# Kernel tuning notes

Hardware: AMD Instinct MI355X
Metric: run time of the kernel (lower is better)

The kernel has to match this reference:

```python
import jax, jax.numpy as jnp
import numpy as np

B, L, D, H = 2, 2048, 1024, 16
DH = D // H  # per-head dim = 64


def setup_inputs() -> dict:
    key = jax.random.key(0)
    ks = jax.random.split(key, 7)
    s = 1.0 / np.sqrt(D)
    x = jax.random.normal(ks[0], (B, L, D), dtype=jnp.float32)
    Wq = jax.random.normal(ks[1], (D, D), dtype=jnp.float32) * s
    bq = jax.random.normal(ks[2], (D,), dtype=jnp.float32) * s
    Wk = jax.random.normal(ks[3], (D, D), dtype=jnp.float32) * s
    bk = jax.random.normal(ks[4], (D,), dtype=jnp.float32) * s
    Wv = jax.random.normal(ks[5], (D, D), dtype=jnp.float32) * s
    bv = jax.random.normal(ks[6], (D,), dtype=jnp.float32) * s
    # strict upper-triangular causal mask; mask==1 means position is masked (-inf)
    atten_mask = jnp.triu(jnp.ones((L, L), dtype=jnp.int32), k=1)
    return {"x": x, "atten_mask": atten_mask, "Wq": Wq, "bq": bq,
            "Wk": Wk, "bk": bk, "Wv": Wv, "bv": bv}


def reference(x, atten_mask, Wq, bq, Wk, bk, Wv, bv):
    # nn.Linear: y = x @ W^T + b
    q = x @ Wq.T + bq  # [B,L,D]
    k = x @ Wk.T + bk
    v = x @ Wv.T + bv
    # contiguous split into heads == reshape to [B,L,H,DH]
    q = q.reshape(B, L, H, DH)
    k = k.reshape(B, L, H, DH)
    v = v.reshape(B, L, H, DH)
    scale = jnp.sqrt(jnp.float32(DH))
    scores = jnp.einsum('blhd,bmhd->bhlm', q, k) / scale  # [B,H,L,L]
    # torch.where(mask == 1, -inf, scores)
    scores = jnp.where(atten_mask[None, None] == 1, -jnp.inf, scores)
    attn = jax.nn.softmax(scores, axis=-1)
    out = jnp.einsum('bhlm,bmhd->blhd', attn, v)  # [B,L,H,DH]
    return out.reshape(B, L, D)  # concat heads along channel dim
```

## Files before the change

kernel.cpp:

```cpp
#include <hip/hip_runtime.h>
#include <hip/hip_bf16.h>

#define BDIM 2
#define LSEQ 2048
#define DMODEL 1024
#define NH 16
#define DHEAD 64
#define CTS 136

typedef __bf16 bf16_t;
typedef __attribute__((ext_vector_type(8))) __bf16 bf16x8;
typedef __attribute__((ext_vector_type(4))) __bf16 bf16x4;
typedef __attribute__((ext_vector_type(2))) __bf16 bf16x2;
typedef __attribute__((ext_vector_type(4))) float f32x4;
typedef __attribute__((ext_vector_type(4))) int i32x4;

static __device__ __forceinline__ f32x4 mfma16(bf16x8 a, bf16x8 b, f32x4 c) {
    return __builtin_amdgcn_mfma_f32_16x16x32_bf16(a, b, c, 0, 0, 0);
}

static __device__ __forceinline__ void load_lds16(const bf16_t* g, void* l) {
    __builtin_amdgcn_global_load_lds(
        (const __attribute__((address_space(1))) void*)g,
        (__attribute__((address_space(3))) void*)l, 16, 0, 0);
}

__global__ void convert_all(
    const float* __restrict__ x,
    const float* __restrict__ Wq, const float* __restrict__ Wk, const float* __restrict__ Wv,
    const float* __restrict__ bq, const float* __restrict__ bk, const float* __restrict__ bv,
    bf16_t* __restrict__ cx,
    bf16_t* __restrict__ cWq, bf16_t* __restrict__ cWk, bf16_t* __restrict__ cWv,
    bf16_t* __restrict__ cbq, bf16_t* __restrict__ cbk, bf16_t* __restrict__ cbv,
    float SQ)
{
    const int blk = blockIdx.x;
    const float* src; bf16_t* dst; int base, cnt; float sc = 1.0f;
    if (blk < 1024)      { src = x;  dst = cx;  base = blk * 1024;          cnt = 1024; }
    else if (blk < 1280) { src = Wq; dst = cWq; base = (blk - 1024) * 1024; cnt = 1024; sc = SQ; }
    else if (blk < 1536) { src = Wk; dst = cWk; base = (blk - 1280) * 1024; cnt = 1024; }
    else if (blk < 1792) { src = Wv; dst = cWv; base = (blk - 1536) * 1024; cnt = 1024; }
    else if (blk == 1792){ src = bq; dst = cbq; base = 0; cnt = 256; sc = SQ; }
    else if (blk == 1793){ src = bk; dst = cbk; base = 0; cnt = 256; }
    else                 { src = bv; dst = cbv; base = 0; cnt = 256; }

    for (int i = base + threadIdx.x; i < base + cnt; i += 256) {
        f32x4 v = *(const f32x4*)(src + 4 * (size_t)i);
        bf16x4 o;
        o[0] = (bf16_t)(v[0] * sc); o[1] = (bf16_t)(v[1] * sc);
        o[2] = (bf16_t)(v[2] * sc); o[3] = (bf16_t)(v[3] * sc);
        *(bf16x4*)(dst + 4 * (size_t)i) = o;
    }
}

__global__ __launch_bounds__(256) void qkv_gemm(
    const bf16_t* __restrict__ x,
    const bf16_t* __restrict__ W0, const bf16_t* __restrict__ W1, const bf16_t* __restrict__ W2,
    const bf16_t* __restrict__ b0, const bf16_t* __restrict__ b1, const bf16_t* __restrict__ b2,
    bf16_t* __restrict__ yq, bf16_t* __restrict__ yk, bf16_t* __restrict__ yvT)
{
    __shared__ alignas(16) char smem[128 * CTS * 2];
    bf16_t* At = (bf16_t*)smem;
    bf16_t* Bt = At + 128 * 64;
    bf16_t* Ct = (bf16_t*)smem;

    const int tid  = threadIdx.x;
    const int lane = tid & 63;
    const int w    = tid >> 6;
    const int quad = lane >> 4;
    const int n16  = lane & 15;
    const int lane3 = lane >> 3;
    const int lane7 = lane & 7;
    const int swz8  = (lane7 ^ lane3) * 8;

    const int m0 = blockIdx.y * 128;
    const int n0 = blockIdx.x * 128;
    const int z  = blockIdx.z;

    const bf16_t* W    = (z == 0) ? W0 : ((z == 1) ? W1 : W2);
    const bf16_t* bias = (z == 0) ? b0 : ((z == 1) ? b1 : b2);

    const int wm = (w >> 1) * 64;
    const int wn = (w & 1) * 64;

    f32x4 acc[4][4] = {};

    const bf16_t* gx = x + (size_t)(m0 + 32 * w + lane3) * DMODEL + swz8;
    const bf16_t* gw = W + (size_t)(n0 + 32 * w + lane3) * DMODEL + swz8;
    char* lA = (char*)At + w * 4096;
    char* lB = (char*)Bt + w * 4096;

    const int swz = n16 & 7;

    for (int k0 = 0; k0 < DMODEL; k0 += 64) {
        #pragma unroll
        for (int ii = 0; ii < 4; ++ii) {
            load_lds16(gx + (size_t)(8 * ii) * DMODEL + k0, lA + ii * 1024);
            load_lds16(gw + (size_t)(8 * ii) * DMODEL + k0, lB + ii * 1024);
        }
        __syncthreads();

        #pragma unroll
        for (int kk = 0; kk < 2; ++kk) {
            bf16x8 af[4], bfv[4];
            #pragma unroll
            for (int mt = 0; mt < 4; ++mt) {
                const bf16_t* ar = At + (wm + mt * 16 + n16) * 64;
                af[mt] = *(const bf16x8*)(ar + (((quad + 4 * kk)) ^ swz) * 8);
            }
            #pragma unroll
            for (int nt = 0; nt < 4; ++nt) {
                const bf16_t* br = Bt + (wn + nt * 16 + n16) * 64;
                bfv[nt] = *(const bf16x8*)(br + (((quad + 4 * kk)) ^ swz) * 8);
            }
            #pragma unroll
            for (int mt = 0; mt < 4; ++mt)
                #pragma unroll
                for (int nt = 0; nt < 4; ++nt)
                    acc[mt][nt] = mfma16(af[mt], bfv[nt], acc[mt][nt]);
        }
        __syncthreads();
    }

    if (z < 2) {
        bf16_t* y = (z == 0) ? yq : yk;
        #pragma unroll
        for (int nt = 0; nt < 4; ++nt) {
            int jc = wn + nt * 16 + n16;
            float bv = (float)bias[n0 + jc];
            #pragma unroll
            for (int mt = 0; mt < 4; ++mt) {
                int rr = wm + mt * 16 + quad * 4;
                #pragma unroll
                for (int r = 0; r < 4; ++r)
                    Ct[(rr + r) * CTS + jc] = (bf16_t)(acc[mt][nt][r] + bv);
            }
        }
        __syncthreads();
        const int l    = tid >> 1;
        const int half = tid & 1;
        const int hh   = (n0 >> 6) + half;
        const int i    = m0 + l;
        const int bb   = i >> 11, ll = i & 2047;
        bf16_t* dst = &y[(((size_t)bb * NH + hh) * LSEQ + ll) * DHEAD];
        const bf16_t* srcr = &Ct[l * CTS + half * 64];
        #pragma unroll
        for (int c = 0; c < 8; ++c)
            *(bf16x8*)(dst + c * 8) = *(const bf16x8*)(srcr + c * 8);
    } else {
        #pragma unroll
        for (int nt = 0; nt < 4; ++nt) {
            int j = n0 + wn + nt * 16 + n16;
            float bv = (float)bias[j];
            #pragma unroll
            for (int mt = 0; mt < 4; ++mt) {
                int i0 = m0 + wm + mt * 16 + quad * 4;
                int bb = i0 >> 11, l = i0 & 2047;
                bf16x4 pk;
                #pragma unroll
                for (int r = 0; r < 4; ++r) pk[r] = (bf16_t)(acc[mt][nt][r] + bv);
                *(bf16x4*)(&yvT[((size_t)bb * DMODEL + j) * LSEQ + l]) = pk;
            }
        }
    }
}

__global__ __launch_bounds__(256) void attn_fused(
    const bf16_t* __restrict__ qp,
    const bf16_t* __restrict__ kp,
    const bf16_t* __restrict__ vtp,
    float* __restrict__ out,
    float* __restrict__ Opart,
    float* __restrict__ ml)
{
    __shared__ alignas(16) bf16_t Ks[2][64 * 64];
    __shared__ alignas(16) bf16_t Vs[2][64 * 64];

    const int tid  = threadIdx.x;
    const int lane = tid & 63;
    const int w    = tid >> 6;
    const int quad = lane >> 4;
    const int n16  = lane & 15;
    const int lane3 = lane >> 3;
    const int lane7 = lane & 7;
    const int swz8  = (lane7 ^ lane3) * 8;
    const int swz   = n16 & 7;

    const int bh  = blockIdx.x;
    const int yy  = blockIdx.y;
    const int p   = yy & 15;
    const bool isA = (yy < 16);
    const int b = bh >> 4, h = bh & 15;
    const int row = w * 16 + n16;
    const size_t hb = (size_t)bh * (LSEQ * DHEAD);

    float m_, l_;
    f32x4 oacc[4];

    auto process = [&](int qt, int t0, int ntiles, bool maskLast) {
        const int iq = qt * 64 + row;
        const bf16_t* qq = qp + hb + (size_t)iq * DHEAD;
        const bf16x8 qb0 = *(const bf16x8*)(qq + quad * 8);
        const bf16x8 qb1 = *(const bf16x8*)(qq + 32 + quad * 8);

        const bf16_t* gk = kp  + hb + (size_t)(t0 * 64 + 16 * w + lane3) * DHEAD + swz8;
        const bf16_t* gv = vtp + hb + (size_t)(16 * w + lane3) * LSEQ + t0 * 64 + swz8;

        int buf = 0;
        {
            char* lk = (char*)&Ks[0][0] + w * 2048;
            char* lv = (char*)&Vs[0][0] + w * 2048;
            load_lds16(gk,              lk);
            load_lds16(gk + 8 * DHEAD,  lk + 1024);
            load_lds16(gv,              lv);
            load_lds16(gv + 8 * LSEQ,   lv + 1024);
            gk += 64 * DHEAD; gv += 64;
        }
        __syncthreads();

        for (int it = 0; it < ntiles; ++it) {
            if (it + 1 < ntiles) {
                char* lk = (char*)&Ks[buf ^ 1][0] + w * 2048;
                char* lv = (char*)&Vs[buf ^ 1][0] + w * 2048;
                load_lds16(gk,              lk);
                load_lds16(gk + 8 * DHEAD,  lk + 1024);
                load_lds16(gv,              lv);
                load_lds16(gv + 8 * LSEQ,   lv + 1024);
                gk += 64 * DHEAD; gv += 64;
            }

            const bf16_t* kb = &Ks[buf][0];
            f32x4 s[4];
            #pragma unroll
            for (int t = 0; t < 4; ++t) {
                const bf16_t* krow = kb + (t * 16 + n16) * 64;
                bf16x8 k0v = *(const bf16x8*)(krow + ((quad    ) ^ swz) * 8);
                bf16x8 k1v = *(const bf16x8*)(krow + ((quad + 4) ^ swz) * 8);
                f32x4 z = {0.f, 0.f, 0.f, 0.f};
                z = mfma16(k0v, qb0, z);
                z = mfma16(k1v, qb1, z);
                s[t] = z;
            }

            if (maskLast && it == ntiles - 1) {
                const int k0 = (t0 + it) * 64;
                #pragma unroll
                for (int t = 0; t < 4; ++t)
                    #pragma unroll
                    for (int r = 0; r < 4; ++r)
                        if (k0 + t * 16 + quad * 4 + r > iq) s[t][r] = -1e30f;
            }

            float mx = -1e30f;
            #pragma unroll
            for (int t = 0; t < 4; ++t)
                mx = fmaxf(mx, fmaxf(fmaxf(s[t][0], s[t][1]), fmaxf(s[t][2], s[t][3])));
            mx = fmaxf(mx, __shfl_xor(mx, 16, 64));
            mx = fmaxf(mx, __shfl_xor(mx, 32, 64));
            const float mnew  = fmaxf(m_, mx);
            const float alpha = __builtin_amdgcn_exp2f(m_ - mnew);
            m_ = mnew;

            float rs = 0.f;
            int pr[4][2];
            #pragma unroll
            for (int t = 0; t < 4; ++t) {
                float p0 = __builtin_amdgcn_exp2f(s[t][0] - mnew);
                float p1 = __builtin_amdgcn_exp2f(s[t][1] - mnew);
                float p2 = __builtin_amdgcn_exp2f(s[t][2] - mnew);
                float p3 = __builtin_amdgcn_exp2f(s[t][3] - mnew);
                rs += (p0 + p1) + (p2 + p3);
                bf16x2 a; a[0] = (bf16_t)p0; a[1] = (bf16_t)p1;
                bf16x2 c; c[0] = (bf16_t)p2; c[1] = (bf16_t)p3;
                pr[t][0] = __builtin_bit_cast(int, a);
                pr[t][1] = __builtin_bit_cast(int, c);
            }
            rs += __shfl_xor(rs, 16, 64);
            rs += __shfl_xor(rs, 32, 64);
            l_ = l_ * alpha + rs;
            #pragma unroll
            for (int t = 0; t < 4; ++t) {
                oacc[t][0] *= alpha; oacc[t][1] *= alpha;
                oacc[t][2] *= alpha; oacc[t][3] *= alpha;
            }

            const bf16_t* vbs = &Vs[buf][0];
            #pragma unroll
            for (int c = 0; c < 2; ++c) {
                int frag[4];
                #pragma unroll
                for (int pi = 0; pi < 4; ++pi) {
                    int srcl = ((((quad & 1) * 2) + (pi >> 1)) * 16 + n16) * 4;
                    int vA = __builtin_amdgcn_ds_bpermute(srcl, pr[2 * c][pi & 1]);
                    int vB = __builtin_amdgcn_ds_bpermute(srcl, pr[2 * c + 1][pi & 1]);
                    frag[pi] = (quad < 2) ? vA : vB;
                }
                i32x4 fv = {frag[0], frag[1], frag[2], frag[3]};
                bf16x8 pb = __builtin_bit_cast(bf16x8, fv);

                #pragma unroll
                for (int t = 0; t < 4; ++t) {
                    const bf16_t* vrow = vbs + (t * 16 + n16) * 64;
                    bf16x8 va = *(const bf16x8*)(vrow + ((quad + 4 * c) ^ swz) * 8);
                    oacc[t] = mfma16(va, pb, oacc[t]);
                }
            }

            __syncthreads();
            buf ^= 1;
        }
    };

    if (isA) {
        m_ = -1e30f; l_ = 0.f;
        #pragma unroll
        for (int t = 0; t < 4; ++t) { f32x4 zz = {0.f,0.f,0.f,0.f}; oacc[t] = zz; }
        process(p, 0, p + 1, true);
        {
            const float inv = 1.0f / l_;
            const int iq = p * 64 + row;
            float* orow = out + ((size_t)b * LSEQ + iq) * DMODEL + h * DHEAD;
            #pragma unroll
            for (int t = 0; t < 4; ++t) {
                f32x4 o;
                o[0] = oacc[t][0] * inv; o[1] = oacc[t][1] * inv;
                o[2] = oacc[t][2] * inv; o[3] = oacc[t][3] * inv;
                *(f32x4*)(orow + t * 16 + quad * 4) = o;
            }
        }
        m_ = -1e30f; l_ = 0.f;
        #pragma unroll
        for (int t = 0; t < 4; ++t) { f32x4 zz = {0.f,0.f,0.f,0.f}; oacc[t] = zz; }
        process(31 - p, 0, 16 - p, false);
        {
            const int pidx = (bh * 16 + (15 - p)) * 2 + 0;
            float* Ob = Opart + (size_t)pidx * 4096 + row * 64;
            #pragma unroll
            for (int t = 0; t < 4; ++t)
                *(f32x4*)(Ob + t * 16 + quad * 4) = oacc[t];
            if (quad == 0) {
                ml[(size_t)pidx * 128 + row * 2]     = m_;
                ml[(size_t)pidx * 128 + row * 2 + 1] = l_;
            }
        }
    } else {
        m_ = -1e30f; l_ = 0.f;
        #pragma unroll
        for (int t = 0; t < 4; ++t) { f32x4 zz = {0.f,0.f,0.f,0.f}; oacc[t] = zz; }
        process(31 - p, 16 - p, 16, true);
        {
            const int pidx = (bh * 16 + (15 - p)) * 2 + 1;
            float* Ob = Opart + (size_t)pidx * 4096 + row * 64;
            #pragma unroll
            for (int t = 0; t < 4; ++t)
                *(f32x4*)(Ob + t * 16 + quad * 4) = oacc[t];
            if (quad == 0) {
                ml[(size_t)pidx * 128 + row * 2]     = m_;
                ml[(size_t)pidx * 128 + row * 2 + 1] = l_;
            }
        }
    }
}

__global__ __launch_bounds__(256) void attn_combine(
    const float* __restrict__ Opart, const float* __restrict__ ml,
    float* __restrict__ out)
{
    const int bh  = blockIdx.x;
    const int q16 = blockIdx.y;
    const int t   = threadIdx.x;
    const int row = t >> 2;
    const int dh0 = (t & 3) * 16;
    const int p0  = (bh * 16 + q16) * 2;
    const int b = bh >> 4, h = bh & 15;

    float m0 = ml[(size_t)p0 * 128 + row * 2];
    float l0 = ml[(size_t)p0 * 128 + row * 2 + 1];
    float m1 = ml[(size_t)(p0 + 1) * 128 + row * 2];
    float l1 = ml[(size_t)(p0 + 1) * 128 + row * 2 + 1];
    float m  = fmaxf(m0, m1);
    float a0 = __builtin_amdgcn_exp2f(m0 - m);
    float a1 = __builtin_amdgcn_exp2f(m1 - m);
    float inv = 1.0f / (a0 * l0 + a1 * l1);
    a0 *= inv; a1 *= inv;

    const float* P0 = Opart + (size_t)p0 * 4096 + row * 64 + dh0;
    const float* P1 = P0 + 4096;
    float* orow = out + ((size_t)b * LSEQ + ((16 + q16) * 64 + row)) * DMODEL
                + h * DHEAD + dh0;
    #pragma unroll
    for (int c = 0; c < 4; ++c) {
        f32x4 o0 = *(const f32x4*)(P0 + 4 * c);
        f32x4 o1 = *(const f32x4*)(P1 + 4 * c);
        f32x4 o;
        o[0] = a0 * o0[0] + a1 * o1[0];
        o[1] = a0 * o0[1] + a1 * o1[1];
        o[2] = a0 * o0[2] + a1 * o1[2];
        o[3] = a0 * o0[3] + a1 * o1[3];
        *(f32x4*)(orow + 4 * c) = o;
    }
}

extern "C" void kernel_launch(void* const* d_in, const int* in_sizes, int n_in,
                              void* d_out, int out_size, void* d_ws, size_t ws_size,
                              hipStream_t stream)
{
    const float* x  = (const float*)d_in[0];
    const float* Wq = (const float*)d_in[2];
    const float* bq = (const float*)d_in[3];
    const float* Wk = (const float*)d_in[4];
    const float* bk = (const float*)d_in[5];
    const float* Wv = (const float*)d_in[6];
    const float* bv = (const float*)d_in[7];
    float* out = (float*)d_out;

    char* ws = (char*)d_ws;
    bf16_t* q   = (bf16_t*)(ws);
    bf16_t* k   = (bf16_t*)(ws + 8u  * 1024 * 1024);
    bf16_t* vT  = (bf16_t*)(ws + 16u * 1024 * 1024);
    bf16_t* cx  = (bf16_t*)(ws + 24u * 1024 * 1024);
    bf16_t* cWq = (bf16_t*)(ws + 32u * 1024 * 1024);
    bf16_t* cWk = (bf16_t*)(ws + 34u * 1024 * 1024);
    bf16_t* cWv = (bf16_t*)(ws + 36u * 1024 * 1024);
    bf16_t* cbq = (bf16_t*)(ws + 38u * 1024 * 1024);
    bf16_t* cbk = (bf16_t*)(ws + 38u * 1024 * 1024 + 4096);
    bf16_t* cbv = (bf16_t*)(ws + 38u * 1024 * 1024 + 8192);
    float*  mlp = (float*) (ws + 39u * 1024 * 1024);
    float*  Op  = (float*) (ws + 40u * 1024 * 1024);

    const float SQ = 0.125f * 1.44269504088896f;

    convert_all<<<1795, 256, 0, stream>>>(x, Wq, Wk, Wv, bq, bk, bv,
                                          cx, cWq, cWk, cWv, cbq, cbk, cbv, SQ);

    dim3 g1(DMODEL / 128, (BDIM * LSEQ) / 128, 3);
    qkv_gemm<<<g1, 256, 0, stream>>>(cx, cWq, cWk, cWv, cbq, cbk, cbv, q, k, vT);

    dim3 g2(BDIM * NH, 32, 1);
    attn_fused<<<g2, 256, 0, stream>>>(q, k, vT, out, Op, mlp);

    dim3 g3(BDIM * NH, 16, 1);
    attn_combine<<<g3, 256, 0, stream>>>(Op, mlp, out);
}
```

Measured before the change: 193.2 us.

## Enlarge attention query tile to 128 rows so each K/V tile serves two groups

Each wave now handles two 16-row query groups, which doubles the query tile per block from 64 to 128 rows. Every K/V tile loaded into LDS, and every K/V fragment read from it, is reused for twice as many MFMAs, cutting K/V traffic per unit of work. The causal split and the combine kernel are reworked for 128-row tiles, and masking now covers the last two KV tiles. The trade-off is half as many blocks (512 instead of 1024) and higher register pressure from doubled accumulators, which may lower occupancy and load balance on a 256-CU part.

```diff
diff --git a/kernel.cpp b/kernel.cpp
--- a/kernel.cpp
+++ b/kernel.cpp
@@ -188,20 +188,24 @@
 
     const int bh  = blockIdx.x;
     const int yy  = blockIdx.y;
-    const int p   = yy & 15;
-    const bool isA = (yy < 16);
+    const int p   = yy & 7;
+    const bool isA = (yy < 8);
     const int b = bh >> 4, h = bh & 15;
-    const int row = w * 16 + n16;
     const size_t hb = (size_t)bh * (LSEQ * DHEAD);
 
-    float m_, l_;
-    f32x4 oacc[4];
-
-    auto process = [&](int qt, int t0, int ntiles, bool maskLast) {
-        const int iq = qt * 64 + row;
-        const bf16_t* qq = qp + hb + (size_t)iq * DHEAD;
-        const bf16x8 qb0 = *(const bf16x8*)(qq + quad * 8);
-        const bf16x8 qb1 = *(const bf16x8*)(qq + 32 + quad * 8);
+    float m_[2], l_[2];
+    f32x4 oacc[2][4];
+
+    auto process = [&](int qt, int t0, int ntiles, bool maskTail) {
+        int iqg[2];
+        bf16x8 qb[2][2];
+        #pragma unroll
+        for (int g = 0; g < 2; ++g) {
+            iqg[g] = qt * 128 + 32 * w + 16 * g + n16;
+            const bf16_t* qq = qp + hb + (size_t)iqg[g] * DHEAD;
+            qb[g][0] = *(const bf16x8*)(qq + quad * 8);
+            qb[g][1] = *(const bf16x8*)(qq + 32 + quad * 8);
+        }
 
         const bf16_t* gk = kp  + hb + (size_t)(t0 * 64 + 16 * w + lane3) * DHEAD + swz8;
         const bf16_t* gv = vtp + hb + (size_t)(16 * w + lane3) * LSEQ + t0 * 64 + swz8;
@@ -210,10 +214,10 @@
         {
             char* lk = (char*)&Ks[0][0] + w * 2048;
             char* lv = (char*)&Vs[0][0] + w * 2048;
-            load_lds16(gk,              lk);
-            load_lds16(gk + 8 * DHEAD,  lk + 1024);
-            load_lds16(gv,              lv);
-            load_lds16(gv + 8 * LSEQ,   lv + 1024);
+            load_lds16(gk,             lk);
+            load_lds16(gk + 8 * DHEAD, lk + 1024);
+            load_lds16(gv,             lv);
+            load_lds16(gv + 8 * LSEQ,  lv + 1024);
             gk += 64 * DHEAD; gv += 64;
         }
         __syncthreads();
@@ -222,87 +226,101 @@
             if (it + 1 < ntiles) {
                 char* lk = (char*)&Ks[buf ^ 1][0] + w * 2048;
                 char* lv = (char*)&Vs[buf ^ 1][0] + w * 2048;
-                load_lds16(gk,              lk);
-                load_lds16(gk + 8 * DHEAD,  lk + 1024);
-                load_lds16(gv,              lv);
-                load_lds16(gv + 8 * LSEQ,   lv + 1024);
+                load_lds16(gk,             lk);
+                load_lds16(gk + 8 * DHEAD, lk + 1024);
+                load_lds16(gv,             lv);
+                load_lds16(gv + 8 * LSEQ,  lv + 1024);
                 gk += 64 * DHEAD; gv += 64;
             }
 
             const bf16_t* kb = &Ks[buf][0];
-            f32x4 s[4];
+            f32x4 s[2][4];
             #pragma unroll
             for (int t = 0; t < 4; ++t) {
                 const bf16_t* krow = kb + (t * 16 + n16) * 64;
                 bf16x8 k0v = *(const bf16x8*)(krow + ((quad    ) ^ swz) * 8);
                 bf16x8 k1v = *(const bf16x8*)(krow + ((quad + 4) ^ swz) * 8);
-                f32x4 z = {0.f, 0.f, 0.f, 0.f};
-                z = mfma16(k0v, qb0, z);
-                z = mfma16(k1v, qb1, z);
-                s[t] = z;
-            }
-
-            if (maskLast && it == ntiles - 1) {
+                #pragma unroll
+                for (int g = 0; g < 2; ++g) {
+                    f32x4 z = {0.f, 0.f, 0.f, 0.f};
+                    z = mfma16(k0v, qb[g][0], z);
+                    z = mfma16(k1v, qb[g][1], z);
+                    s[g][t] = z;
+                }
+            }
+
+            if (maskTail && it >= ntiles - 2) {
                 const int k0 = (t0 + it) * 64;
                 #pragma unroll
+                for (int g = 0; g < 2; ++g)
+                    #pragma unroll
+                    for (int t = 0; t < 4; ++t)
+                        #pragma unroll
+                        for (int r = 0; r < 4; ++r)
+                            if (k0 + t * 16 + quad * 4 + r > iqg[g]) s[g][t][r] = -1e30f;
+            }
+
+            bf16x8 pb[2][2];
+            #pragma unroll
+            for (int g = 0; g < 2; ++g) {
+                float mx = -1e30f;
+                #pragma unroll
                 for (int t = 0; t < 4; ++t)
+                    mx = fmaxf(mx, fmaxf(fmaxf(s[g][t][0], s[g][t][1]),
+                                         fmaxf(s[g][t][2], s[g][t][3])));
+                mx = fmaxf(mx, __shfl_xor(mx, 16, 64));
+                mx = fmaxf(mx, __shfl_xor(mx, 32, 64));
+                const float mnew  = fmaxf(m_[g], mx);
+                const float alpha = __builtin_amdgcn_exp2f(m_[g] - mnew);
+                m_[g] = mnew;
+
+                float rs = 0.f;
+                int pr[4][2];
+                #pragma unroll
+                for (int t = 0; t < 4; ++t) {
+                    float p0 = __builtin_amdgcn_exp2f(s[g][t][0] - mnew);
+                    float p1 = __builtin_amdgcn_exp2f(s[g][t][1] - mnew);
+                    float p2 = __builtin_amdgcn_exp2f(s[g][t][2] - mnew);
+                    float p3 = __builtin_amdgcn_exp2f(s[g][t][3] - mnew);
+                    rs += (p0 + p1) + (p2 + p3);
+                    bf16x2 a; a[0] = (bf16_t)p0; a[1] = (bf16_t)p1;
+                    bf16x2 c; c[0] = (bf16_t)p2; c[1] = (bf16_t)p3;
+                    pr[t][0] = __builtin_bit_cast(int, a);
+                    pr[t][1] = __builtin_bit_cast(int, c);
+                }
+                rs += __shfl_xor(rs, 16, 64);
+                rs += __shfl_xor(rs, 32, 64);
+                l_[g] = l_[g] * alpha + rs;
+                #pragma unroll
+                for (int t = 0; t < 4; ++t) {
+                    oacc[g][t][0] *= alpha; oacc[g][t][1] *= alpha;
+                    oacc[g][t][2] *= alpha; oacc[g][t][3] *= alpha;
+                }
+
+                #pragma unroll
+                for (int c = 0; c < 2; ++c) {
+                    int frag[4];
                     #pragma unroll
-                    for (int r = 0; r < 4; ++r)
-                        if (k0 + t * 16 + quad * 4 + r > iq) s[t][r] = -1e30f;
-            }
-
-            float mx = -1e30f;
-            #pragma unroll
-            for (int t = 0; t < 4; ++t)
-                mx = fmaxf(mx, fmaxf(fmaxf(s[t][0], s[t][1]), fmaxf(s[t][2], s[t][3])));
-            mx = fmaxf(mx, __shfl_xor(mx, 16, 64));
-            mx = fmaxf(mx, __shfl_xor(mx, 32, 64));
-            const float mnew  = fmaxf(m_, mx);
-            const float alpha = __builtin_amdgcn_exp2f(m_ - mnew);
-            m_ = mnew;
-
-            float rs = 0.f;
-            int pr[4][2];
-            #pragma unroll
-            for (int t = 0; t < 4; ++t) {
-                float p0 = __builtin_amdgcn_exp2f(s[t][0] - mnew);
-                float p1 = __builtin_amdgcn_exp2f(s[t][1] - mnew);
-                float p2 = __builtin_amdgcn_exp2f(s[t][2] - mnew);
-                float p3 = __builtin_amdgcn_exp2f(s[t][3] - mnew);
-                rs += (p0 + p1) + (p2 + p3);
-                bf16x2 a; a[0] = (bf16_t)p0; a[1] = (bf16_t)p1;
-                bf16x2 c; c[0] = (bf16_t)p2; c[1] = (bf16_t)p3;
-                pr[t][0] = __builtin_bit_cast(int, a);
-                pr[t][1] = __builtin_bit_cast(int, c);
-            }
-            rs += __shfl_xor(rs, 16, 64);
-            rs += __shfl_xor(rs, 32, 64);
-            l_ = l_ * alpha + rs;
-            #pragma unroll
-            for (int t = 0; t < 4; ++t) {
-                oacc[t][0] *= alpha; oacc[t][1] *= alpha;
-                oacc[t][2] *= alpha; oacc[t][3] *= alpha;
+                    for (int pi = 0; pi < 4; ++pi) {
+                        int srcl = ((((quad & 1) * 2) + (pi >> 1)) * 16 + n16) * 4;
+                        int vA = __builtin_amdgcn_ds_bpermute(srcl, pr[2 * c][pi & 1]);
+                        int vB = __builtin_amdgcn_ds_bpermute(srcl, pr[2 * c + 1][pi & 1]);
+                        frag[pi] = (quad < 2) ? vA : vB;
+                    }
+                    i32x4 fv = {frag[0], frag[1], frag[2], frag[3]};
+                    pb[g][c] = __builtin_bit_cast(bf16x8, fv);
+                }
             }
 
             const bf16_t* vbs = &Vs[buf][0];
             #pragma unroll
             for (int c = 0; c < 2; ++c) {
-                int frag[4];
-                #pragma unroll
-                for (int pi = 0; pi < 4; ++pi) {
-                    int srcl = ((((quad & 1) * 2) + (pi >> 1)) * 16 + n16) * 4;
-                    int vA = __builtin_amdgcn_ds_bpermute(srcl, pr[2 * c][pi & 1]);
-                    int vB = __builtin_amdgcn_ds_bpermute(srcl, pr[2 * c + 1][pi & 1]);
-                    frag[pi] = (quad < 2) ? vA : vB;
-                }
-                i32x4 fv = {frag[0], frag[1], frag[2], frag[3]};
-                bf16x8 pb = __builtin_bit_cast(bf16x8, fv);
-
                 #pragma unroll
                 for (int t = 0; t < 4; ++t) {
                     const bf16_t* vrow = vbs + (t * 16 + n16) * 64;
                     bf16x8 va = *(const bf16x8*)(vrow + ((quad + 4 * c) ^ swz) * 8);
-                    oacc[t] = mfma16(va, pb, oacc[t]);
+                    oacc[0][t] = mfma16(va, pb[0][c], oacc[0][t]);
+                    oacc[1][t] = mfma16(va, pb[1][c], oacc[1][t]);
                 }
             }
 
@@ -311,54 +329,53 @@
         }
     };
 
+    auto zero_state = [&]() {
+        #pragma unroll
+        for (int g = 0; g < 2; ++g) {
+            m_[g] = -1e30f; l_[g] = 0.f;
+            #pragma unroll
+            for (int t = 0; t < 4; ++t) { f32x4 zz = {0.f,0.f,0.f,0.f}; oacc[g][t] = zz; }
+        }
+    };
+
+    auto store_partial = [&](int pidx) {
+        #pragma unroll
+        for (int g = 0; g < 2; ++g) {
+            const int row = 32 * w + 16 * g + n16;
+            float* Ob = Opart + (size_t)pidx * (128 * 64) + row * 64;
+            #pragma unroll
+            for (int t = 0; t < 4; ++t)
+                *(f32x4*)(Ob + t * 16 + quad * 4) = oacc[g][t];
+            if (quad == 0) {
+                ml[(size_t)pidx * 256 + row * 2]     = m_[g];
+                ml[(size_t)pidx * 256 + row * 2 + 1] = l_[g];
+            }
+        }
+    };
+
     if (isA) {
-        m_ = -1e30f; l_ = 0.f;
-        #pragma unroll
-        for (int t = 0; t < 4; ++t) { f32x4 zz = {0.f,0.f,0.f,0.f}; oacc[t] = zz; }
-        process(p, 0, p + 1, true);
-        {
-            const float inv = 1.0f / l_;
-            const int iq = p * 64 + row;
+        zero_state();
+        process(p, 0, 2 * p + 2, true);
+        #pragma unroll
+        for (int g = 0; g < 2; ++g) {
+            const float inv = 1.0f / l_[g];
+            const int iq = p * 128 + 32 * w + 16 * g + n16;
             float* orow = out + ((size_t)b * LSEQ + iq) * DMODEL + h * DHEAD;
             #pragma unroll
             for (int t = 0; t < 4; ++t) {
                 f32x4 o;
-                o[0] = oacc[t][0] * inv; o[1] = oacc[t][1] * inv;
-                o[2] = oacc[t][2] * inv; o[3] = oacc[t][3] * inv;
+                o[0] = oacc[g][t][0] * inv; o[1] = oacc[g][t][1] * inv;
+                o[2] = oacc[g][t][2] * inv; o[3] = oacc[g][t][3] * inv;
                 *(f32x4*)(orow + t * 16 + quad * 4) = o;
             }
         }
-        m_ = -1e30f; l_ = 0.f;
-        #pragma unroll
-        for (int t = 0; t < 4; ++t) { f32x4 zz = {0.f,0.f,0.f,0.f}; oacc[t] = zz; }
-        process(31 - p, 0, 16 - p, false);
-        {
-            const int pidx = (bh * 16 + (15 - p)) * 2 + 0;
-            float* Ob = Opart + (size_t)pidx * 4096 + row * 64;
-            #pragma unroll
-            for (int t = 0; t < 4; ++t)
-                *(f32x4*)(Ob + t * 16 + quad * 4) = oacc[t];
-            if (quad == 0) {
-                ml[(size_t)pidx * 128 + row * 2]     = m_;
-                ml[(size_t)pidx * 128 + row * 2 + 1] = l_;
-            }
-        }
+        zero_state();
+        process(15 - p, 0, 15 - 2 * p, false);
+        store_partial((bh * 8 + (7 - p)) * 2 + 0);
     } else {
-        m_ = -1e30f; l_ = 0.f;
-        #pragma unroll
-        for (int t = 0; t < 4; ++t) { f32x4 zz = {0.f,0.f,0.f,0.f}; oacc[t] = zz; }
-        process(31 - p, 16 - p, 16, true);
-        {
-            const int pidx = (bh * 16 + (15 - p)) * 2 + 1;
-            float* Ob = Opart + (size_t)pidx * 4096 + row * 64;
-            #pragma unroll
-            for (int t = 0; t < 4; ++t)
-                *(f32x4*)(Ob + t * 16 + quad * 4) = oacc[t];
-            if (quad == 0) {
-                ml[(size_t)pidx * 128 + row * 2]     = m_;
-                ml[(size_t)pidx * 128 + row * 2 + 1] = l_;
-            }
-        }
+        zero_state();
+        process(15 - p, 15 - 2 * p, 17, true);
+        store_partial((bh * 8 + (7 - p)) * 2 + 1);
     }
 }
 
@@ -366,30 +383,30 @@
     const float* __restrict__ Opart, const float* __restrict__ ml,
     float* __restrict__ out)
 {
-    const int bh  = blockIdx.x;
-    const int q16 = blockIdx.y;
-    const int t   = threadIdx.x;
-    const int row = t >> 2;
-    const int dh0 = (t & 3) * 16;
-    const int p0  = (bh * 16 + q16) * 2;
+    const int bh = blockIdx.x;
+    const int q8 = blockIdx.y;
+    const int t  = threadIdx.x;
+    const int row = t >> 1;
+    const int dh0 = (t & 1) * 32;
+    const int p0  = (bh * 8 + q8) * 2;
     const int b = bh >> 4, h = bh & 15;
 
-    float m0 = ml[(size_t)p0 * 128 + row * 2];
-    float l0 = ml[(size_t)p0 * 128 + row * 2 + 1];
-    float m1 = ml[(size_t)(p0 + 1) * 128 + row * 2];
-    float l1 = ml[(size_t)(p0 + 1) * 128 + row * 2 + 1];
+    float m0 = ml[(size_t)p0 * 256 + row * 2];
+    float l0 = ml[(size_t)p0 * 256 + row * 2 + 1];
+    float m1 = ml[(size_t)(p0 + 1) * 256 + row * 2];
+    float l1 = ml[(size_t)(p0 + 1) * 256 + row * 2 + 1];
     float m  = fmaxf(m0, m1);
     float a0 = __builtin_amdgcn_exp2f(m0 - m);
     float a1 = __builtin_amdgcn_exp2f(m1 - m);
     float inv = 1.0f / (a0 * l0 + a1 * l1);
     a0 *= inv; a1 *= inv;
 
-    const float* P0 = Opart + (size_t)p0 * 4096 + row * 64 + dh0;
-    const float* P1 = P0 + 4096;
-    float* orow = out + ((size_t)b * LSEQ + ((16 + q16) * 64 + row)) * DMODEL
+    const float* P0 = Opart + (size_t)p0 * (128 * 64) + row * 64 + dh0;
+    const float* P1 = P0 + 128 * 64;
+    float* orow = out + ((size_t)b * LSEQ + ((8 + q8) * 128 + row)) * DMODEL
                 + h * DHEAD + dh0;
     #pragma unroll
-    for (int c = 0; c < 4; ++c) {
+    for (int c = 0; c < 8; ++c) {
         f32x4 o0 = *(const f32x4*)(P0 + 4 * c);
         f32x4 o1 = *(const f32x4*)(P1 + 4 * c);
         f32x4 o;
@@ -436,9 +453,9 @@
     dim3 g1(DMODEL / 128, (BDIM * LSEQ) / 128, 3);
     qkv_gemm<<<g1, 256, 0, stream>>>(cx, cWq, cWk, cWv, cbq, cbk, cbv, q, k, vT);
 
-    dim3 g2(BDIM * NH, 32, 1);
+    dim3 g2(BDIM * NH, 16, 1);
     attn_fused<<<g2, 256, 0, stream>>>(q, k, vT, out, Op, mlp);
 
-    dim3 g3(BDIM * NH, 16, 1);
+    dim3 g3(BDIM * NH, 8, 1);
     attn_combine<<<g3, 256, 0, stream>>>(Op, mlp, out);
 }
```

Result: no change. 191.1 us (-1.1%).
